# Kernel optimization log

Hardware: AMD Instinct MI355X
Metric: run time of the kernel (lower is better)

Reference implementation:

```python
import jax, jax.numpy as jnp
import numpy as np

N = 100000      # nodes
E = 800000      # edges (avg degree 8)
D_IN = 64
H1 = H2 = H3 = 64
HEADS = 2
D_EDGE = 5
NEG_SLOPE = 0.2  # GATConv leaky_relu slope


def _lin(key, fi, fo):
    kw, kb = jax.random.split(key)
    w = jax.random.normal(kw, (fi, fo), jnp.float32) / np.sqrt(fi)
    b = jax.random.normal(kb, (fo,), jnp.float32) * 0.01
    return w, b


def setup_inputs() -> dict:
    key = jax.random.key(0)
    ks = jax.random.split(key, 16)
    x = jax.random.normal(ks[0], (N, D_IN), jnp.float32)
    edge_index = jax.random.randint(ks[1], (2, E), 0, N, dtype=jnp.int32)
    edge_attr = jax.random.normal(ks[2], (E, D_EDGE), jnp.float32)

    inp = {"x": x, "edge_index": edge_index, "edge_attr": edge_attr}
    dims = [(D_IN, H1), (H1, H2), (H2, H3)]
    for i, (fi, fo) in enumerate(dims, start=1):
        k = jax.random.fold_in(ks[3], i)
        ka, kb, kc = jax.random.split(k, 3)
        inp[f"w_node{i}"], inp[f"b_node{i}"] = _lin(ka, fi, fo)
        inp[f"w_edge{i}"], inp[f"b_edge{i}"] = _lin(kb, D_EDGE, fo)
        inp[f"w_comb{i}"], inp[f"b_comb{i}"] = _lin(kc, 2 * fo, fo)
    # GATConv: shared lin for src/dst, att vectors, bias (concat=False -> size H3)
    kg, ks_, kd, kbias = jax.random.split(ks[4], 4)
    inp["w_gat"] = jax.random.normal(kg, (H3, HEADS * H3), jnp.float32) / np.sqrt(H3)
    inp["att_src"] = jax.random.normal(ks_, (HEADS, H3), jnp.float32) * 0.1
    inp["att_dst"] = jax.random.normal(kd, (HEADS, H3), jnp.float32) * 0.1
    inp["b_gat"] = jax.random.normal(kbias, (H3,), jnp.float32) * 0.01
    return inp


def _edge_conv(h, src, dst, ea, wn, bn, we, be, wc, bc, n):
    # lin_node / lin_edge applied densely, then gather -> concat -> lin -> scatter-add
    hn = h @ wn + bn                       # [N, C]
    ef = ea @ we + be                      # [E, C]
    msg = jnp.concatenate([hn[src], ef], axis=1) @ wc + bc  # [E, C]
    return jax.ops.segment_sum(msg, dst, num_segments=n)


def _gat(h, src, dst, w_gat, att_src, att_dst, b_gat, n):
    g = (h @ w_gat).reshape(n, HEADS, -1)          # [N, H, C]
    a_src = jnp.einsum("nhc,hc->nh", g, att_src)    # [N, H]
    a_dst = jnp.einsum("nhc,hc->nh", g, att_dst)
    alpha = jax.nn.leaky_relu(a_src[src] + a_dst[dst], NEG_SLOPE)  # [E, H]
    # segment softmax over incoming edges of each dst node
    m = jax.ops.segment_max(alpha, dst, num_segments=n)
    alpha = jnp.exp(alpha - m[dst])
    denom = jax.ops.segment_sum(alpha, dst, num_segments=n)
    alpha = alpha / (denom[dst] + 1e-16)
    out = jax.ops.segment_sum(g[src] * alpha[:, :, None], dst, num_segments=n)  # [N,H,C]
    return out.mean(axis=1) + b_gat  # concat=False -> mean over heads, plus bias


def reference(x, edge_index, edge_attr,
              w_node1, b_node1, w_edge1, b_edge1, w_comb1, b_comb1,
              w_node2, b_node2, w_edge2, b_edge2, w_comb2, b_comb2,
              w_node3, b_node3, w_edge3, b_edge3, w_comb3, b_comb3,
              w_gat, att_src, att_dst, b_gat):
    n = x.shape[0]
    src, dst = edge_index[0], edge_index[1]
    h = x
    h = jax.nn.relu(_edge_conv(h, src, dst, edge_attr, w_node1, b_node1, w_edge1, b_edge1, w_comb1, b_comb1, n))
    h = jax.nn.relu(_edge_conv(h, src, dst, edge_attr, w_node2, b_node2, w_edge2, b_edge2, w_comb2, b_comb2, n))
    h = jax.nn.relu(_edge_conv(h, src, dst, edge_attr, w_node3, b_node3, w_edge3, b_edge3, w_comb3, b_comb3, n))
    h = _gat(h, src, dst, w_gat, att_src, att_dst, b_gat, n)
    return h.reshape(-1)  # torch.flatten
```

## Files before the change

### kernel.cpp

```cpp
#include <hip/hip_runtime.h>
#include <hip/hip_fp16.h>
#include <math.h>


#define TPB 256

typedef unsigned int u32;

__device__ inline float2 f16unpack2(u32 u) {
    __half2 h = *reinterpret_cast<__half2*>(&u);
    return __half22float2(h);
}
__device__ inline float4 f16unpack4(uint2 q) {
    float2 a = f16unpack2(q.x), b = f16unpack2(q.y);
    return make_float4(a.x, a.y, b.x, b.y);
}
__device__ inline u32 f16pack2(float lo, float hi) {
    __half2 h = __floats2half2_rn(lo, hi);
    return *reinterpret_cast<u32*>(&h);
}
__device__ inline void acc_h16(float4& acc, uint2 v) {
    float2 a = f16unpack2(v.x);
    float2 b = f16unpack2(v.y);
    acc.x += a.x; acc.y += a.y; acc.z += b.x; acc.w += b.y;
}

#define MAC4(acc, a, w0, w1, w2, w3)                                           \
    acc.x = fmaf(a.x, w0.x, acc.x); acc.y = fmaf(a.x, w0.y, acc.y);            \
    acc.z = fmaf(a.x, w0.z, acc.z); acc.w = fmaf(a.x, w0.w, acc.w);            \
    acc.x = fmaf(a.y, w1.x, acc.x); acc.y = fmaf(a.y, w1.y, acc.y);            \
    acc.z = fmaf(a.y, w1.z, acc.z); acc.w = fmaf(a.y, w1.w, acc.w);            \
    acc.x = fmaf(a.z, w2.x, acc.x); acc.y = fmaf(a.z, w2.y, acc.y);            \
    acc.z = fmaf(a.z, w2.z, acc.z); acc.w = fmaf(a.z, w2.w, acc.w);            \
    acc.x = fmaf(a.w, w3.x, acc.x); acc.y = fmaf(a.w, w3.y, acc.y);            \
    acc.z = fmaf(a.w, w3.z, acc.z); acc.w = fmaf(a.w, w3.w, acc.w);

struct CombPtrs {
    const float* wn; const float* bn;
    const float* we; const float* be;
    const float* wc; const float* bc;
    float* W1;
};

__global__ __launch_bounds__(TPB) void k_prep(CombPtrs p0, CombPtrs p1, CombPtrs p2,
                                              const float* __restrict__ wg, u32* __restrict__ wgh,
                                              const float* __restrict__ att_src,
                                              const float* __restrict__ att_dst,
                                              float* __restrict__ vsd,
                                              const float4* __restrict__ X, uint4* __restrict__ XH,
                                              int n8, int nbC,
                                              int* __restrict__ rs, int nz) {
    const int b = blockIdx.x;
    if (b >= 4 + nbC) {
        int i = (b - 4 - nbC) * TPB + threadIdx.x;
        if (i < nz) rs[i] = 0;
        return;
    }
    if (b >= 4) {
        int i = (b - 4) * TPB + threadIdx.x;
        if (i < n8) {
            float4 a = X[i * 2], c = X[i * 2 + 1];
            uint4 o;
            o.x = f16pack2(a.x, a.y); o.y = f16pack2(a.z, a.w);
            o.z = f16pack2(c.x, c.y); o.w = f16pack2(c.z, c.w);
            XH[i] = o;
        }
        return;
    }
    if (b == 3) {
        for (int i = threadIdx.x; i < 4096; i += TPB) {
            float2 v = *(const float2*)&wg[i * 2];
            wgh[i] = f16pack2(v.x, v.y);
        }
        {
            int i = threadIdx.x;
            int type = i >> 6, k = i & 63;
            int h = type & 1, sd = type >> 1;
            const float* att = (sd ? att_dst : att_src) + h * 64;
            const float* wrow = wg + k * 128 + h * 64;
            float acc = 0.f;
            #pragma unroll 8
            for (int c = 0; c < 64; c++) acc = fmaf(wrow[c], att[c], acc);
            vsd[type * 64 + k] = acc;
        }
        return;
    }
    CombPtrs P = (b == 0) ? p0 : ((b == 1) ? p1 : p2);
    const float* wn = P.wn; const float* bn = P.bn;
    const float* we = P.we; const float* be = P.be;
    const float* wc = P.wc; const float* bc = P.bc;
    float* W1 = P.W1;
    float* W2 = P.W1 + 4096;
    float* cv = P.W1 + 4416;
    int tid = threadIdx.x;
    for (int idx = tid; idx < 64 * 64; idx += TPB) {
        int i = idx >> 6, j = idx & 63;
        float acc = 0.f;
        #pragma unroll 8
        for (int k = 0; k < 64; k++) acc = fmaf(wn[i * 64 + k], wc[k * 64 + j], acc);
        W1[idx] = acc;
    }
    for (int idx = tid; idx < 5 * 64; idx += TPB) {
        int i = idx >> 6, j = idx & 63;
        float acc = 0.f;
        #pragma unroll 8
        for (int k = 0; k < 64; k++) acc = fmaf(we[i * 64 + k], wc[(64 + k) * 64 + j], acc);
        W2[idx] = acc;
    }
    for (int j = tid; j < 64; j += TPB) {
        float acc = bc[j];
        for (int k = 0; k < 64; k++) {
            acc = fmaf(bn[k], wc[k * 64 + j], acc);
            acc = fmaf(be[k], wc[(64 + k) * 64 + j], acc);
        }
        cv[j] = acc;
    }
}

__global__ __launch_bounds__(TPB) void k_hist(const int* __restrict__ dst, int* __restrict__ cnt,
                                              int* __restrict__ rank, int E) {
    int e = blockIdx.x * TPB + threadIdx.x;
    if (e < E) rank[e] = atomicAdd(&cnt[dst[e]], 1);
}

__global__ __launch_bounds__(TPB) void k_scan1(int* __restrict__ data, int* __restrict__ partials, int n) {
    __shared__ int s[TPB];
    int i = blockIdx.x * TPB + threadIdx.x;
    int v = (i < n) ? data[i] : 0;
    s[threadIdx.x] = v;
    __syncthreads();
    for (int off = 1; off < TPB; off <<= 1) {
        int t = (threadIdx.x >= off) ? s[threadIdx.x - off] : 0;
        __syncthreads();
        s[threadIdx.x] += t;
        __syncthreads();
    }
    if (i < n) data[i] = s[threadIdx.x] - v;
    if (threadIdx.x == TPB - 1) partials[blockIdx.x] = s[TPB - 1];
}

__global__ __launch_bounds__(TPB) void k_scan3(int* __restrict__ data, const int* __restrict__ partials,
                                               int n, int total) {
    const int bid = blockIdx.x;
    int s = 0;
    for (int j = threadIdx.x; j < bid; j += TPB) s += partials[j];
    #pragma unroll
    for (int off = 32; off > 0; off >>= 1) s += __shfl_down(s, off);
    __shared__ int ws[4];
    if ((threadIdx.x & 63) == 0) ws[threadIdx.x >> 6] = s;
    __syncthreads();
    int pre = ws[0] + ws[1] + ws[2] + ws[3];
    int i = bid * TPB + threadIdx.x;
    if (i < n) data[i] += pre;
    if (i == 0) data[n] = total;
}

__global__ __launch_bounds__(TPB) void k_scatter(const int* __restrict__ src, const int* __restrict__ dst,
                                                 const int* __restrict__ rank, const int* __restrict__ row_start,
                                                 int2* __restrict__ csr_se, int E) {
    int e = blockIdx.x * TPB + threadIdx.x;
    if (e < E) {
        int idx = row_start[dst[e]] + rank[e];
        csr_se[idx] = make_int2(src[e], e);
    }
}

template <bool IN16, bool OUT16, bool SCORES, bool B5C>
__global__ __launch_bounds__(TPB, 6) void k_ec_fused(const void* __restrict__ Hv,
                                                     const int* __restrict__ row_start,
                                                     const int2* __restrict__ csr_se,
                                                     const float* __restrict__ Wfold,
                                                     float* __restrict__ B5,
                                                     const float* __restrict__ EA,
                                                     void* __restrict__ OUTv, int n,
                                                     const float* __restrict__ vsd,
                                                     float* __restrict__ asrc,
                                                     float* __restrict__ adst) {
    __shared__ float Alds[64 * 68];
    __shared__ float Blds[B5C ? 320 : 4];
    const float* Hf = (const float*)Hv;
    const u32*   Hh = (const u32*)Hv;
    const int t = threadIdx.x;
    const int base = blockIdx.x * 64;

    const int lane = t & 63;
    const int lid = lane & 15;
    const int gbase = lane & 48;
    const int gid = t >> 4;
    const int c4 = lid * 4;
    const int h2i = lid * 2;
    for (int i = 0; i < 4; i++) {
        int r = gid * 4 + i;
        int node = base + r;
        float4 acc = make_float4(0.f, 0.f, 0.f, 0.f);
        float b0 = 0.f, b1 = 0.f, b2 = 0.f, b3 = 0.f, b4 = 0.f;
        if (node < n) {
            int beg = row_start[node], end = row_start[node + 1];
            for (int chunk = beg; chunk < end; chunk += 16) {
                int cdeg = min(end - chunk, 16);
                bool ev = (chunk + lid < end);
                int2 se = ev ? csr_se[chunk + lid] : make_int2(0, 0);
                int s_l = se.x;
                if (B5C && ev) {
                    const float* p = EA + (size_t)se.y * 5;
                    b0 += p[0]; b1 += p[1]; b2 += p[2]; b3 += p[3]; b4 += p[4];
                }
                int it = 0;
                for (; it + 7 < cdeg; it += 8) {
                    int se0 = __shfl(s_l, gbase + it);
                    int se1 = __shfl(s_l, gbase + it + 1);
                    int se2 = __shfl(s_l, gbase + it + 2);
                    int se3 = __shfl(s_l, gbase + it + 3);
                    int se4 = __shfl(s_l, gbase + it + 4);
                    int se5 = __shfl(s_l, gbase + it + 5);
                    int se6 = __shfl(s_l, gbase + it + 6);
                    int se7 = __shfl(s_l, gbase + it + 7);
                    if (IN16) {
                        uint2 v0 = *(const uint2*)&Hh[(size_t)se0 * 32 + h2i];
                        uint2 v1 = *(const uint2*)&Hh[(size_t)se1 * 32 + h2i];
                        uint2 v2 = *(const uint2*)&Hh[(size_t)se2 * 32 + h2i];
                        uint2 v3 = *(const uint2*)&Hh[(size_t)se3 * 32 + h2i];
                        uint2 v4 = *(const uint2*)&Hh[(size_t)se4 * 32 + h2i];
                        uint2 v5 = *(const uint2*)&Hh[(size_t)se5 * 32 + h2i];
                        uint2 v6 = *(const uint2*)&Hh[(size_t)se6 * 32 + h2i];
                        uint2 v7 = *(const uint2*)&Hh[(size_t)se7 * 32 + h2i];
                        acc_h16(acc, v0); acc_h16(acc, v1); acc_h16(acc, v2); acc_h16(acc, v3);
                        acc_h16(acc, v4); acc_h16(acc, v5); acc_h16(acc, v6); acc_h16(acc, v7);
                    } else {
                        float4 v0 = *(const float4*)&Hf[(size_t)se0 * 64 + c4];
                        float4 v1 = *(const float4*)&Hf[(size_t)se1 * 64 + c4];
                        float4 v2 = *(const float4*)&Hf[(size_t)se2 * 64 + c4];
                        float4 v3 = *(const float4*)&Hf[(size_t)se3 * 64 + c4];
                        float4 v4 = *(const float4*)&Hf[(size_t)se4 * 64 + c4];
                        float4 v5 = *(const float4*)&Hf[(size_t)se5 * 64 + c4];
                        float4 v6 = *(const float4*)&Hf[(size_t)se6 * 64 + c4];
                        float4 v7 = *(const float4*)&Hf[(size_t)se7 * 64 + c4];
                        acc.x += ((v0.x + v1.x) + (v2.x + v3.x)) + ((v4.x + v5.x) + (v6.x + v7.x));
                        acc.y += ((v0.y + v1.y) + (v2.y + v3.y)) + ((v4.y + v5.y) + (v6.y + v7.y));
                        acc.z += ((v0.z + v1.z) + (v2.z + v3.z)) + ((v4.z + v5.z) + (v6.z + v7.z));
                        acc.w += ((v0.w + v1.w) + (v2.w + v3.w)) + ((v4.w + v5.w) + (v6.w + v7.w));
                    }
                }
                for (; it + 3 < cdeg; it += 4) {
                    int se0 = __shfl(s_l, gbase + it);
                    int se1 = __shfl(s_l, gbase + it + 1);
                    int se2 = __shfl(s_l, gbase + it + 2);
                    int se3 = __shfl(s_l, gbase + it + 3);
                    if (IN16) {
                        uint2 v0 = *(const uint2*)&Hh[(size_t)se0 * 32 + h2i];
                        uint2 v1 = *(const uint2*)&Hh[(size_t)se1 * 32 + h2i];
                        uint2 v2 = *(const uint2*)&Hh[(size_t)se2 * 32 + h2i];
                        uint2 v3 = *(const uint2*)&Hh[(size_t)se3 * 32 + h2i];
                        acc_h16(acc, v0); acc_h16(acc, v1); acc_h16(acc, v2); acc_h16(acc, v3);
                    } else {
                        float4 v0 = *(const float4*)&Hf[(size_t)se0 * 64 + c4];
                        float4 v1 = *(const float4*)&Hf[(size_t)se1 * 64 + c4];
                        float4 v2 = *(const float4*)&Hf[(size_t)se2 * 64 + c4];
                        float4 v3 = *(const float4*)&Hf[(size_t)se3 * 64 + c4];
                        acc.x += (v0.x + v1.x) + (v2.x + v3.x);
                        acc.y += (v0.y + v1.y) + (v2.y + v3.y);
                        acc.z += (v0.z + v1.z) + (v2.z + v3.z);
                        acc.w += (v0.w + v1.w) + (v2.w + v3.w);
                    }
                }
                for (; it < cdeg; it++) {
                    int se_ = __shfl(s_l, gbase + it);
                    if (IN16) {
                        uint2 v = *(const uint2*)&Hh[(size_t)se_ * 32 + h2i];
                        acc_h16(acc, v);
                    } else {
                        float4 v = *(const float4*)&Hf[(size_t)se_ * 64 + c4];
                        acc.x += v.x; acc.y += v.y; acc.z += v.z; acc.w += v.w;
                    }
                }
            }
        }
        *(float4*)&Alds[r * 68 + c4] = acc;
        if (B5C) {
            #pragma unroll
            for (int off = 1; off < 16; off <<= 1) {
                b0 += __shfl_xor(b0, off); b1 += __shfl_xor(b1, off);
                b2 += __shfl_xor(b2, off); b3 += __shfl_xor(b3, off);
                b4 += __shfl_xor(b4, off);
            }
            if (lid == 0 && node < n) {
                Blds[r * 5 + 0] = b0; Blds[r * 5 + 1] = b1; Blds[r * 5 + 2] = b2;
                Blds[r * 5 + 3] = b3; Blds[r * 5 + 4] = b4;
                float* bp = B5 + (size_t)node * 5;
                bp[0] = b0; bp[1] = b1; bp[2] = b2; bp[3] = b3; bp[4] = b4;
            }
        }
    }
    __syncthreads();

    const int r0 = (t >> 4) * 4, c0 = (t & 15) * 4;
    float4 acc0 = make_float4(0.f, 0.f, 0.f, 0.f), acc1 = acc0, acc2 = acc0, acc3 = acc0;
    #pragma unroll 2
    for (int k = 0; k < 64; k += 4) {
        float4 a0 = *(float4*)&Alds[(r0 + 0) * 68 + k];
        float4 a1 = *(float4*)&Alds[(r0 + 1) * 68 + k];
        float4 a2 = *(float4*)&Alds[(r0 + 2) * 68 + k];
        float4 a3 = *(float4*)&Alds[(r0 + 3) * 68 + k];
        float4 w0 = *(const float4*)&Wfold[(k + 0) * 64 + c0];
        float4 w1 = *(const float4*)&Wfold[(k + 1) * 64 + c0];
        float4 w2 = *(const float4*)&Wfold[(k + 2) * 64 + c0];
        float4 w3 = *(const float4*)&Wfold[(k + 3) * 64 + c0];
        MAC4(acc0, a0, w0, w1, w2, w3);
        MAC4(acc1, a1, w0, w1, w2, w3);
        MAC4(acc2, a2, w0, w1, w2, w3);
        MAC4(acc3, a3, w0, w1, w2, w3);
    }
    float4 w2c[5];
    #pragma unroll
    for (int j = 0; j < 5; j++) w2c[j] = *(const float4*)&Wfold[4096 + j * 64 + c0];
    const float4 cv4 = *(const float4*)&Wfold[4416 + c0];
    float4 vs0, vs1, vd0, vd1;
    if (SCORES) {
        vs0 = *(const float4*)&vsd[0 * 64 + c0];
        vs1 = *(const float4*)&vsd[1 * 64 + c0];
        vd0 = *(const float4*)&vsd[2 * 64 + c0];
        vd1 = *(const float4*)&vsd[3 * 64 + c0];
    }

    #define DOT4(a, b) (a.x * b.x + a.y * b.y + a.z * b.z + a.w * b.w)
    #define EC_STORE(i, acc)                                                        \
        { int row = base + r0 + i;                                                  \
          if (row < n) {                                                            \
              float deg = (float)(row_start[row + 1] - row_start[row]);             \
              float4 q;                                                             \
              q.x = deg * cv4.x; q.y = deg * cv4.y;                                 \
              q.z = deg * cv4.z; q.w = deg * cv4.w;                                 \
              for (int j = 0; j < 5; j++) {                                         \
                  float b = B5C ? Blds[(r0 + i) * 5 + j] : B5[(size_t)row * 5 + j]; \
                  q.x = fmaf(b, w2c[j].x, q.x); q.y = fmaf(b, w2c[j].y, q.y);       \
                  q.z = fmaf(b, w2c[j].z, q.z); q.w = fmaf(b, w2c[j].w, q.w);       \
              }                                                                     \
              float4 r4;                                                            \
              r4.x = fmaxf(acc.x + q.x, 0.f); r4.y = fmaxf(acc.y + q.y, 0.f);       \
              r4.z = fmaxf(acc.z + q.z, 0.f); r4.w = fmaxf(acc.w + q.w, 0.f);       \
              if (SCORES) {                                                         \
                  float s0 = DOT4(r4, vs0), s1 = DOT4(r4, vs1);                     \
                  float d0 = DOT4(r4, vd0), d1 = DOT4(r4, vd1);                     \
                  s0 += __shfl_xor(s0, 1); s1 += __shfl_xor(s1, 1);                 \
                  d0 += __shfl_xor(d0, 1); d1 += __shfl_xor(d1, 1);                 \
                  s0 += __shfl_xor(s0, 2); s1 += __shfl_xor(s1, 2);                 \
                  d0 += __shfl_xor(d0, 2); d1 += __shfl_xor(d1, 2);                 \
                  s0 += __shfl_xor(s0, 4); s1 += __shfl_xor(s1, 4);                 \
                  d0 += __shfl_xor(d0, 4); d1 += __shfl_xor(d1, 4);                 \
                  s0 += __shfl_xor(s0, 8); s1 += __shfl_xor(s1, 8);                 \
                  d0 += __shfl_xor(d0, 8); d1 += __shfl_xor(d1, 8);                 \
                  if ((t & 15) == 0) {                                              \
                      float2 sv; sv.x = s0; sv.y = s1;                              \
                      float2 dv; dv.x = d0; dv.y = d1;                              \
                      *(float2*)&asrc[(size_t)row * 2] = sv;                        \
                      *(float2*)&adst[(size_t)row * 2] = dv;                        \
                  }                                                                 \
              }                                                                     \
              if (OUT16) {                                                          \
                  u32* O = (u32*)OUTv;                                              \
                  uint2 gg;                                                         \
                  gg.x = f16pack2(r4.x, r4.y); gg.y = f16pack2(r4.z, r4.w);         \
                  *(uint2*)&O[(size_t)row * 32 + (c0 >> 1)] = gg;                   \
              } else {                                                              \
                  float* O = (float*)OUTv;                                          \
                  *(float4*)&O[(size_t)row * 64 + c0] = r4;                         \
              } } }
    EC_STORE(0, acc0) EC_STORE(1, acc1) EC_STORE(2, acc2) EC_STORE(3, acc3)
    #undef EC_STORE
    #undef DOT4
}

__global__ __launch_bounds__(TPB) void k_gat_agg(const u32* __restrict__ Hh,
                                                 const int* __restrict__ row_start,
                                                 const int2* __restrict__ csr_se,
                                                 const float* __restrict__ asrc,
                                                 const float* __restrict__ adst,
                                                 const u32* __restrict__ Wgh,
                                                 const float* __restrict__ bgat,
                                                 float* __restrict__ OUT, int n) {
    __shared__ float Ash[16][2][68];
    const int t = threadIdx.x;
    const int g = t >> 4;
    const int node = blockIdx.x * 16 + g;
    const int lane = t & 63;
    const int lid = lane & 15;
    const int gbase = lane & 48;
    const int h2i = lid * 2;
    const bool active = (node < n);

    float m0 = -INFINITY, m1 = -INFINITY, d0 = 0.f, d1 = 0.f;
    float A0[4] = {0.f, 0.f, 0.f, 0.f};
    float A1[4] = {0.f, 0.f, 0.f, 0.f};
    int beg = 0, end = 0;
    float2 adv = make_float2(0.f, 0.f);
    if (active) {
        beg = row_start[node]; end = row_start[node + 1];
        adv = *(const float2*)&adst[(size_t)node * 2];
    }
    for (int chunk = beg; chunk < end; chunk += 16) {
        int cdeg = min(end - chunk, 16);
        bool valid = (lid < cdeg);
        int s_l = valid ? csr_se[chunk + lid].x : 0;
        float al0 = -INFINITY, al1 = -INFINITY;
        if (valid) {
            float2 av = *(const float2*)&asrc[(size_t)s_l * 2];
            float t0 = av.x + adv.x, t1 = av.y + adv.y;
            al0 = (t0 > 0.f) ? t0 : 0.2f * t0;
            al1 = (t1 > 0.f) ? t1 : 0.2f * t1;
        }
        float cm0 = al0, cm1 = al1;
        #pragma unroll
        for (int off = 1; off < 16; off <<= 1) {
            cm0 = fmaxf(cm0, __shfl_xor(cm0, off));
            cm1 = fmaxf(cm1, __shfl_xor(cm1, off));
        }
        float nm0 = fmaxf(m0, cm0), nm1 = fmaxf(m1, cm1);
        float sc0 = __expf(m0 - nm0), sc1 = __expf(m1 - nm1);
        float w0 = valid ? __expf(al0 - nm0) : 0.f;
        float w1 = valid ? __expf(al1 - nm1) : 0.f;
        float cd0 = w0, cd1 = w1;
        #pragma unroll
        for (int off = 1; off < 16; off <<= 1) {
            cd0 += __shfl_xor(cd0, off);
            cd1 += __shfl_xor(cd1, off);
        }
        d0 = d0 * sc0 + cd0;
        d1 = d1 * sc1 + cd1;
        #pragma unroll
        for (int j = 0; j < 4; j++) { A0[j] *= sc0; A1[j] *= sc1; }
        m0 = nm0; m1 = nm1;
        int it = 0;
        for (; it + 3 < cdeg; it += 4) {
            int sa = __shfl(s_l, gbase + it);
            int sb = __shfl(s_l, gbase + it + 1);
            int sc = __shfl(s_l, gbase + it + 2);
            int sd = __shfl(s_l, gbase + it + 3);
            float w0a = __shfl(w0, gbase + it),     w1a = __shfl(w1, gbase + it);
            float w0b = __shfl(w0, gbase + it + 1), w1b = __shfl(w1, gbase + it + 1);
            float w0c = __shfl(w0, gbase + it + 2), w1c = __shfl(w1, gbase + it + 2);
            float w0d = __shfl(w0, gbase + it + 3), w1d = __shfl(w1, gbase + it + 3);
            float4 ha = f16unpack4(*(const uint2*)&Hh[(size_t)sa * 32 + h2i]);
            float4 hb = f16unpack4(*(const uint2*)&Hh[(size_t)sb * 32 + h2i]);
            float4 hc = f16unpack4(*(const uint2*)&Hh[(size_t)sc * 32 + h2i]);
            float4 hd = f16unpack4(*(const uint2*)&Hh[(size_t)sd * 32 + h2i]);
            A0[0] = fmaf(w0a, ha.x, A0[0]); A1[0] = fmaf(w1a, ha.x, A1[0]);
            A0[1] = fmaf(w0a, ha.y, A0[1]); A1[1] = fmaf(w1a, ha.y, A1[1]);
            A0[2] = fmaf(w0a, ha.z, A0[2]); A1[2] = fmaf(w1a, ha.z, A1[2]);
            A0[3] = fmaf(w0a, ha.w, A0[3]); A1[3] = fmaf(w1a, ha.w, A1[3]);
            A0[0] = fmaf(w0b, hb.x, A0[0]); A1[0] = fmaf(w1b, hb.x, A1[0]);
            A0[1] = fmaf(w0b, hb.y, A0[1]); A1[1] = fmaf(w1b, hb.y, A1[1]);
            A0[2] = fmaf(w0b, hb.z, A0[2]); A1[2] = fmaf(w1b, hb.z, A1[2]);
            A0[3] = fmaf(w0b, hb.w, A0[3]); A1[3] = fmaf(w1b, hb.w, A1[3]);
            A0[0] = fmaf(w0c, hc.x, A0[0]); A1[0] = fmaf(w1c, hc.x, A1[0]);
            A0[1] = fmaf(w0c, hc.y, A0[1]); A1[1] = fmaf(w1c, hc.y, A1[1]);
            A0[2] = fmaf(w0c, hc.z, A0[2]); A1[2] = fmaf(w1c, hc.z, A1[2]);
            A0[3] = fmaf(w0c, hc.w, A0[3]); A1[3] = fmaf(w1c, hc.w, A1[3]);
            A0[0] = fmaf(w0d, hd.x, A0[0]); A1[0] = fmaf(w1d, hd.x, A1[0]);
            A0[1] = fmaf(w0d, hd.y, A0[1]); A1[1] = fmaf(w1d, hd.y, A1[1]);
            A0[2] = fmaf(w0d, hd.z, A0[2]); A1[2] = fmaf(w1d, hd.z, A1[2]);
            A0[3] = fmaf(w0d, hd.w, A0[3]); A1[3] = fmaf(w1d, hd.w, A1[3]);
        }
        for (; it < cdeg; it++) {
            int sa = __shfl(s_l, gbase + it);
            float w0a = __shfl(w0, gbase + it), w1a = __shfl(w1, gbase + it);
            float4 ha = f16unpack4(*(const uint2*)&Hh[(size_t)sa * 32 + h2i]);
            A0[0] = fmaf(w0a, ha.x, A0[0]); A1[0] = fmaf(w1a, ha.x, A1[0]);
            A0[1] = fmaf(w0a, ha.y, A0[1]); A1[1] = fmaf(w1a, ha.y, A1[1]);
            A0[2] = fmaf(w0a, ha.z, A0[2]); A1[2] = fmaf(w1a, ha.z, A1[2]);
            A0[3] = fmaf(w0a, ha.w, A0[3]); A1[3] = fmaf(w1a, ha.w, A1[3]);
        }
    }
    float r0s = 0.5f / (d0 + 1e-16f);
    float r1s = 0.5f / (d1 + 1e-16f);
    #pragma unroll
    for (int j = 0; j < 4; j++) {
        Ash[g][0][lid * 4 + j] = A0[j] * r0s;
        Ash[g][1][lid * 4 + j] = A1[j] * r1s;
    }
    __syncthreads();

    if (active) {
        const int c0 = (t & 15) * 4;
        const float4 bg = *(const float4*)&bgat[c0];
        float4 acc = bg;
        #pragma unroll 4
        for (int k = 0; k < 64; k++) {
            float a0 = Ash[g][0][k];
            float a1 = Ash[g][1][k];
            float4 w0v = f16unpack4(*(const uint2*)&Wgh[k * 64 + (c0 >> 1)]);
            float4 w1v = f16unpack4(*(const uint2*)&Wgh[k * 64 + 32 + (c0 >> 1)]);
            acc.x = fmaf(a0, w0v.x, acc.x); acc.y = fmaf(a0, w0v.y, acc.y);
            acc.z = fmaf(a0, w0v.z, acc.z); acc.w = fmaf(a0, w0v.w, acc.w);
            acc.x = fmaf(a1, w1v.x, acc.x); acc.y = fmaf(a1, w1v.y, acc.y);
            acc.z = fmaf(a1, w1v.z, acc.z); acc.w = fmaf(a1, w1v.w, acc.w);
        }
        *(float4*)&OUT[(size_t)node * 64 + c0] = acc;
    }
}

extern "C" void kernel_launch(void* const* d_in, const int* in_sizes, int n_in,
                              void* d_out, int out_size, void* d_ws, size_t ws_size,
                              hipStream_t stream) {
    const float* x   = (const float*)d_in[0];
    const int*   ei  = (const int*)d_in[1];
    const float* ea  = (const float*)d_in[2];
    const int N = in_sizes[0] / 64;
    const int E = in_sizes[1] / 2;
    const int* src = ei;
    const int* dst = ei + E;

    const float* wn[3] = {(const float*)d_in[3],  (const float*)d_in[9],  (const float*)d_in[15]};
    const float* bn[3] = {(const float*)d_in[4],  (const float*)d_in[10], (const float*)d_in[16]};
    const float* we[3] = {(const float*)d_in[5],  (const float*)d_in[11], (const float*)d_in[17]};
    const float* be[3] = {(const float*)d_in[6],  (const float*)d_in[12], (const float*)d_in[18]};
    const float* wc[3] = {(const float*)d_in[7],  (const float*)d_in[13], (const float*)d_in[19]};
    const float* bc[3] = {(const float*)d_in[8],  (const float*)d_in[14], (const float*)d_in[20]};
    const float* wgat    = (const float*)d_in[21];
    const float* att_src = (const float*)d_in[22];
    const float* att_dst = (const float*)d_in[23];
    const float* bgat    = (const float*)d_in[24];

    char* ws = (char*)d_ws;
    size_t off = 0;
    auto alloc = [&](size_t bytes) -> void* {
        void* p = ws + off;
        off = (off + bytes + 255) & ~(size_t)255;
        return p;
    };
    int*   row_start = (int*)alloc((size_t)(N + 1) * 4);
    int*   partials  = (int*)alloc(1024 * 4);
    int*   rank      = (int*)alloc((size_t)E * 4);
    int2*  csr_se    = (int2*)alloc((size_t)E * 8);
    float* Wc        = (float*)alloc((size_t)3 * 4480 * 4);
    u32*   Wgh       = (u32*)alloc((size_t)4096 * 4);
    float* vsd       = (float*)alloc((size_t)256 * 4);
    float* B5        = (float*)alloc((size_t)N * 5 * 4);
    u32*   xh        = (u32*)alloc((size_t)N * 64 * 2);
    u32*   bufH0     = (u32*)alloc((size_t)N * 64 * 2);
    u32*   bufH1     = (u32*)alloc((size_t)N * 64 * 2);
    float* asrc      = (float*)alloc((size_t)N * 2 * 4);
    float* adst      = (float*)alloc((size_t)N * 2 * 4);
    float* out = (float*)d_out;

    const int nbN = (N + TPB - 1) / TPB;
    const int nbE = (E + TPB - 1) / TPB;
    const int grpBlocks = (N + 15) / 16;
    const int tiles = (N + 63) / 64;
    const int n8 = N * 8;
    const int nbC = (n8 + TPB - 1) / TPB;
    const int nbZ = (N + 1 + TPB - 1) / TPB;

    CombPtrs p0 = {wn[0], bn[0], we[0], be[0], wc[0], bc[0], Wc};
    CombPtrs p1 = {wn[1], bn[1], we[1], be[1], wc[1], bc[1], Wc + 4480};
    CombPtrs p2 = {wn[2], bn[2], we[2], be[2], wc[2], bc[2], Wc + 2 * 4480};
    k_prep<<<4 + nbC + nbZ, TPB, 0, stream>>>(p0, p1, p2, wgat, Wgh,
                                              att_src, att_dst, vsd,
                                              (const float4*)x, (uint4*)xh, n8, nbC,
                                              row_start, N + 1);

    k_hist<<<nbE, TPB, 0, stream>>>(dst, row_start, rank, E);
    k_scan1<<<nbN, TPB, 0, stream>>>(row_start, partials, N);
    k_scan3<<<nbN, TPB, 0, stream>>>(row_start, partials, N, E);
    k_scatter<<<nbE, TPB, 0, stream>>>(src, dst, rank, row_start, csr_se, E);

    k_ec_fused<true, true, false, true><<<tiles, TPB, 0, stream>>>(
        xh,    row_start, csr_se, Wc,            B5, ea, bufH0, N,
        nullptr, nullptr, nullptr);
    k_ec_fused<true, true, false, false><<<tiles, TPB, 0, stream>>>(
        bufH0, row_start, csr_se, Wc + 4480,     B5, nullptr, bufH1, N,
        nullptr, nullptr, nullptr);
    k_ec_fused<true, true, true, false><<<tiles, TPB, 0, stream>>>(
        bufH1, row_start, csr_se, Wc + 2 * 4480, B5, nullptr, bufH0, N,
        vsd, asrc, adst);

    k_gat_agg<<<grpBlocks, TPB, 0, stream>>>(bufH0, row_start, csr_se, asrc, adst,
                                             Wgh, bgat, out, N);
}
```

Before: 457.9 us.

## Tile GAT aggregation over 64 nodes per block with register-blocked output GEMM

The GAT aggregation kernel now handles 64 nodes per block, with each 16-lane group processing 4 nodes in sequence instead of one. Aggregated features are staged in shared memory as packed fp16, and the final per-head projection is register-blocked: each thread computes 4 rows × 4 columns, so each weight load is reused across four nodes. The gather loop is unrolled to 8 edges with all loads issued before the shuffles, and launch bounds request 6 blocks. The aim is to reduce redundant weight loads and expose more memory-level parallelism, at the cost of serialising nodes within a group and extra fp16 rounding of the intermediate.

```diff
diff --git a/kernel.cpp b/kernel.cpp
--- a/kernel.cpp
+++ b/kernel.cpp
@@ -370,132 +370,164 @@
     #undef DOT4
 }
 
-__global__ __launch_bounds__(TPB) void k_gat_agg(const u32* __restrict__ Hh,
-                                                 const int* __restrict__ row_start,
-                                                 const int2* __restrict__ csr_se,
-                                                 const float* __restrict__ asrc,
-                                                 const float* __restrict__ adst,
-                                                 const u32* __restrict__ Wgh,
-                                                 const float* __restrict__ bgat,
-                                                 float* __restrict__ OUT, int n) {
-    __shared__ float Ash[16][2][68];
+__global__ __launch_bounds__(TPB, 6) void k_gat_agg(const u32* __restrict__ Hh,
+                                                    const int* __restrict__ row_start,
+                                                    const int2* __restrict__ csr_se,
+                                                    const float* __restrict__ asrc,
+                                                    const float* __restrict__ adst,
+                                                    const u32* __restrict__ Wgh,
+                                                    const float* __restrict__ bgat,
+                                                    float* __restrict__ OUT, int n) {
+    __shared__ u32 Ash[64 * 66];
     const int t = threadIdx.x;
-    const int g = t >> 4;
-    const int node = blockIdx.x * 16 + g;
+    const int base = blockIdx.x * 64;
     const int lane = t & 63;
     const int lid = lane & 15;
     const int gbase = lane & 48;
+    const int gid = t >> 4;
     const int h2i = lid * 2;
-    const bool active = (node < n);
-
-    float m0 = -INFINITY, m1 = -INFINITY, d0 = 0.f, d1 = 0.f;
-    float A0[4] = {0.f, 0.f, 0.f, 0.f};
-    float A1[4] = {0.f, 0.f, 0.f, 0.f};
-    int beg = 0, end = 0;
-    float2 adv = make_float2(0.f, 0.f);
-    if (active) {
-        beg = row_start[node]; end = row_start[node + 1];
-        adv = *(const float2*)&adst[(size_t)node * 2];
-    }
-    for (int chunk = beg; chunk < end; chunk += 16) {
-        int cdeg = min(end - chunk, 16);
-        bool valid = (lid < cdeg);
-        int s_l = valid ? csr_se[chunk + lid].x : 0;
-        float al0 = -INFINITY, al1 = -INFINITY;
-        if (valid) {
-            float2 av = *(const float2*)&asrc[(size_t)s_l * 2];
-            float t0 = av.x + adv.x, t1 = av.y + adv.y;
-            al0 = (t0 > 0.f) ? t0 : 0.2f * t0;
-            al1 = (t1 > 0.f) ? t1 : 0.2f * t1;
+
+    #define EDGE_FMA(hv, wa0, wa1)                                              \
+        { float4 hx = f16unpack4(hv);                                           \
+          A0[0] = fmaf(wa0, hx.x, A0[0]); A1[0] = fmaf(wa1, hx.x, A1[0]);       \
+          A0[1] = fmaf(wa0, hx.y, A0[1]); A1[1] = fmaf(wa1, hx.y, A1[1]);       \
+          A0[2] = fmaf(wa0, hx.z, A0[2]); A1[2] = fmaf(wa1, hx.z, A1[2]);       \
+          A0[3] = fmaf(wa0, hx.w, A0[3]); A1[3] = fmaf(wa1, hx.w, A1[3]); }
+
+    for (int i = 0; i < 4; i++) {
+        int r = gid * 4 + i;
+        int node = base + r;
+        float m0 = -INFINITY, m1 = -INFINITY, d0 = 0.f, d1 = 0.f;
+        float A0[4] = {0.f, 0.f, 0.f, 0.f};
+        float A1[4] = {0.f, 0.f, 0.f, 0.f};
+        if (node < n) {
+            int beg = row_start[node], end = row_start[node + 1];
+            float2 adv = *(const float2*)&adst[(size_t)node * 2];
+            for (int chunk = beg; chunk < end; chunk += 16) {
+                int cdeg = min(end - chunk, 16);
+                bool valid = (lid < cdeg);
+                int s_l = valid ? csr_se[chunk + lid].x : 0;
+                float al0 = -INFINITY, al1 = -INFINITY;
+                if (valid) {
+                    float2 av = *(const float2*)&asrc[(size_t)s_l * 2];
+                    float t0 = av.x + adv.x, t1 = av.y + adv.y;
+                    al0 = (t0 > 0.f) ? t0 : 0.2f * t0;
+                    al1 = (t1 > 0.f) ? t1 : 0.2f * t1;
+                }
+                float cm0 = al0, cm1 = al1;
+                #pragma unroll
+                for (int off = 1; off < 16; off <<= 1) {
+                    cm0 = fmaxf(cm0, __shfl_xor(cm0, off));
+                    cm1 = fmaxf(cm1, __shfl_xor(cm1, off));
+                }
+                float nm0 = fmaxf(m0, cm0), nm1 = fmaxf(m1, cm1);
+                float sc0 = __expf(m0 - nm0), sc1 = __expf(m1 - nm1);
+                float w0 = valid ? __expf(al0 - nm0) : 0.f;
+                float w1 = valid ? __expf(al1 - nm1) : 0.f;
+                float cd0 = w0, cd1 = w1;
+                #pragma unroll
+                for (int off = 1; off < 16; off <<= 1) {
+                    cd0 += __shfl_xor(cd0, off);
+                    cd1 += __shfl_xor(cd1, off);
+                }
+                d0 = d0 * sc0 + cd0;
+                d1 = d1 * sc1 + cd1;
+                #pragma unroll
+                for (int j = 0; j < 4; j++) { A0[j] *= sc0; A1[j] *= sc1; }
+                m0 = nm0; m1 = nm1;
+                int it = 0;
+                for (; it + 7 < cdeg; it += 8) {
+                    int s0 = __shfl(s_l, gbase + it);
+                    int s1 = __shfl(s_l, gbase + it + 1);
+                    int s2 = __shfl(s_l, gbase + it + 2);
+                    int s3 = __shfl(s_l, gbase + it + 3);
+                    int s4 = __shfl(s_l, gbase + it + 4);
+                    int s5 = __shfl(s_l, gbase + it + 5);
+                    int s6 = __shfl(s_l, gbase + it + 6);
+                    int s7 = __shfl(s_l, gbase + it + 7);
+                    uint2 v0 = *(const uint2*)&Hh[(size_t)s0 * 32 + h2i];
+                    uint2 v1 = *(const uint2*)&Hh[(size_t)s1 * 32 + h2i];
+                    uint2 v2 = *(const uint2*)&Hh[(size_t)s2 * 32 + h2i];
+                    uint2 v3 = *(const uint2*)&Hh[(size_t)s3 * 32 + h2i];
+                    uint2 v4 = *(const uint2*)&Hh[(size_t)s4 * 32 + h2i];
+                    uint2 v5 = *(const uint2*)&Hh[(size_t)s5 * 32 + h2i];
+                    uint2 v6 = *(const uint2*)&Hh[(size_t)s6 * 32 + h2i];
+                    uint2 v7 = *(const uint2*)&Hh[(size_t)s7 * 32 + h2i];
+                    float w00 = __shfl(w0, gbase + it),     w10 = __shfl(w1, gbase + it);
+                    float w01 = __shfl(w0, gbase + it + 1), w11 = __shfl(w1, gbase + it + 1);
+                    float w02 = __shfl(w0, gbase + it + 2), w12 = __shfl(w1, gbase + it + 2);
+                    float w03 = __shfl(w0, gbase + it + 3), w13 = __shfl(w1, gbase + it + 3);
+                    float w04 = __shfl(w0, gbase + it + 4), w14 = __shfl(w1, gbase + it + 4);
+                    float w05 = __shfl(w0, gbase + it + 5), w15 = __shfl(w1, gbase + it + 5);
+                    float w06 = __shfl(w0, gbase + it + 6), w16 = __shfl(w1, gbase + it + 6);
+                    float w07 = __shfl(w0, gbase + it + 7), w17 = __shfl(w1, gbase + it + 7);
+                    EDGE_FMA(v0, w00, w10) EDGE_FMA(v1, w01, w11)
+                    EDGE_FMA(v2, w02, w12) EDGE_FMA(v3, w03, w13)
+                    EDGE_FMA(v4, w04, w14) EDGE_FMA(v5, w05, w15)
+                    EDGE_FMA(v6, w06, w16) EDGE_FMA(v7, w07, w17)
+                }
+                for (; it + 3 < cdeg; it += 4) {
+                    int s0 = __shfl(s_l, gbase + it);
+                    int s1 = __shfl(s_l, gbase + it + 1);
+                    int s2 = __shfl(s_l, gbase + it + 2);
+                    int s3 = __shfl(s_l, gbase + it + 3);
+                    uint2 v0 = *(const uint2*)&Hh[(size_t)s0 * 32 + h2i];
+                    uint2 v1 = *(const uint2*)&Hh[(size_t)s1 * 32 + h2i];
+                    uint2 v2 = *(const uint2*)&Hh[(size_t)s2 * 32 + h2i];
+                    uint2 v3 = *(const uint2*)&Hh[(size_t)s3 * 32 + h2i];
+                    float w00 = __shfl(w0, gbase + it),     w10 = __shfl(w1, gbase + it);
+                    float w01 = __shfl(w0, gbase + it + 1), w11 = __shfl(w1, gbase + it + 1);
+                    float w02 = __shfl(w0, gbase + it + 2), w12 = __shfl(w1, gbase + it + 2);
+                    float w03 = __shfl(w0, gbase + it + 3), w13 = __shfl(w1, gbase + it + 3);
+                    EDGE_FMA(v0, w00, w10) EDGE_FMA(v1, w01, w11)
+                    EDGE_FMA(v2, w02, w12) EDGE_FMA(v3, w03, w13)
+                }
+                for (; it < cdeg; it++) {
+                    int s0 = __shfl(s_l, gbase + it);
+                    uint2 v0 = *(const uint2*)&Hh[(size_t)s0 * 32 + h2i];
+                    float w00 = __shfl(w0, gbase + it), w10 = __shfl(w1, gbase + it);
+                    EDGE_FMA(v0, w00, w10)
+                }
+            }
         }
-        float cm0 = al0, cm1 = al1;
-        #pragma unroll
-        for (int off = 1; off < 16; off <<= 1) {
-            cm0 = fmaxf(cm0, __shfl_xor(cm0, off));
-            cm1 = fmaxf(cm1, __shfl_xor(cm1, off));
-        }
-        float nm0 = fmaxf(m0, cm0), nm1 = fmaxf(m1, cm1);
-        float sc0 = __expf(m0 - nm0), sc1 = __expf(m1 - nm1);
-        float w0 = valid ? __expf(al0 - nm0) : 0.f;
-        float w1 = valid ? __expf(al1 - nm1) : 0.f;
-        float cd0 = w0, cd1 = w1;
-        #pragma unroll
-        for (int off = 1; off < 16; off <<= 1) {
-            cd0 += __shfl_xor(cd0, off);
-            cd1 += __shfl_xor(cd1, off);
-        }
-        d0 = d0 * sc0 + cd0;
-        d1 = d1 * sc1 + cd1;
-        #pragma unroll
-        for (int j = 0; j < 4; j++) { A0[j] *= sc0; A1[j] *= sc1; }
-        m0 = nm0; m1 = nm1;
-        int it = 0;
-        for (; it + 3 < cdeg; it += 4) {
-            int sa = __shfl(s_l, gbase + it);
-            int sb = __shfl(s_l, gbase + it + 1);
-            int sc = __shfl(s_l, gbase + it + 2);
-            int sd = __shfl(s_l, gbase + it + 3);
-            float w0a = __shfl(w0, gbase + it),     w1a = __shfl(w1, gbase + it);
-            float w0b = __shfl(w0, gbase + it + 1), w1b = __shfl(w1, gbase + it + 1);
-            float w0c = __shfl(w0, gbase + it + 2), w1c = __shfl(w1, gbase + it + 2);
-            float w0d = __shfl(w0, gbase + it + 3), w1d = __shfl(w1, gbase + it + 3);
-            float4 ha = f16unpack4(*(const uint2*)&Hh[(size_t)sa * 32 + h2i]);
-            float4 hb = f16unpack4(*(const uint2*)&Hh[(size_t)sb * 32 + h2i]);
-            float4 hc = f16unpack4(*(const uint2*)&Hh[(size_t)sc * 32 + h2i]);
-            float4 hd = f16unpack4(*(const uint2*)&Hh[(size_t)sd * 32 + h2i]);
-            A0[0] = fmaf(w0a, ha.x, A0[0]); A1[0] = fmaf(w1a, ha.x, A1[0]);
-            A0[1] = fmaf(w0a, ha.y, A0[1]); A1[1] = fmaf(w1a, ha.y, A1[1]);
-            A0[2] = fmaf(w0a, ha.z, A0[2]); A1[2] = fmaf(w1a, ha.z, A1[2]);
-            A0[3] = fmaf(w0a, ha.w, A0[3]); A1[3] = fmaf(w1a, ha.w, A1[3]);
-            A0[0] = fmaf(w0b, hb.x, A0[0]); A1[0] = fmaf(w1b, hb.x, A1[0]);
-            A0[1] = fmaf(w0b, hb.y, A0[1]); A1[1] = fmaf(w1b, hb.y, A1[1]);
-            A0[2] = fmaf(w0b, hb.z, A0[2]); A1[2] = fmaf(w1b, hb.z, A1[2]);
-            A0[3] = fmaf(w0b, hb.w, A0[3]); A1[3] = fmaf(w1b, hb.w, A1[3]);
-            A0[0] = fmaf(w0c, hc.x, A0[0]); A1[0] = fmaf(w1c, hc.x, A1[0]);
-            A0[1] = fmaf(w0c, hc.y, A0[1]); A1[1] = fmaf(w1c, hc.y, A1[1]);
-            A0[2] = fmaf(w0c, hc.z, A0[2]); A1[2] = fmaf(w1c, hc.z, A1[2]);
-            A0[3] = fmaf(w0c, hc.w, A0[3]); A1[3] = fmaf(w1c, hc.w, A1[3]);
-            A0[0] = fmaf(w0d, hd.x, A0[0]); A1[0] = fmaf(w1d, hd.x, A1[0]);
-            A0[1] = fmaf(w0d, hd.y, A0[1]); A1[1] = fmaf(w1d, hd.y, A1[1]);
-            A0[2] = fmaf(w0d, hd.z, A0[2]); A1[2] = fmaf(w1d, hd.z, A1[2]);
-            A0[3] = fmaf(w0d, hd.w, A0[3]); A1[3] = fmaf(w1d, hd.w, A1[3]);
-        }
-        for (; it < cdeg; it++) {
-            int sa = __shfl(s_l, gbase + it);
-            float w0a = __shfl(w0, gbase + it), w1a = __shfl(w1, gbase + it);
-            float4 ha = f16unpack4(*(const uint2*)&Hh[(size_t)sa * 32 + h2i]);
-            A0[0] = fmaf(w0a, ha.x, A0[0]); A1[0] = fmaf(w1a, ha.x, A1[0]);
-            A0[1] = fmaf(w0a, ha.y, A0[1]); A1[1] = fmaf(w1a, ha.y, A1[1]);
-            A0[2] = fmaf(w0a, ha.z, A0[2]); A1[2] = fmaf(w1a, ha.z, A1[2]);
-            A0[3] = fmaf(w0a, ha.w, A0[3]); A1[3] = fmaf(w1a, ha.w, A1[3]);
-        }
-    }
-    float r0s = 0.5f / (d0 + 1e-16f);
-    float r1s = 0.5f / (d1 + 1e-16f);
-    #pragma unroll
-    for (int j = 0; j < 4; j++) {
-        Ash[g][0][lid * 4 + j] = A0[j] * r0s;
-        Ash[g][1][lid * 4 + j] = A1[j] * r1s;
-    }
+        float r0s = 0.5f / (d0 + 1e-16f);
+        float r1s = 0.5f / (d1 + 1e-16f);
+        Ash[r * 66 + h2i]          = f16pack2(A0[0] * r0s, A0[1] * r0s);
+        Ash[r * 66 + h2i + 1]      = f16pack2(A0[2] * r0s, A0[3] * r0s);
+        Ash[r * 66 + 32 + h2i]     = f16pack2(A1[0] * r1s, A1[1] * r1s);
+        Ash[r * 66 + 32 + h2i + 1] = f16pack2(A1[2] * r1s, A1[3] * r1s);
+    }
+    #undef EDGE_FMA
     __syncthreads();
 
-    if (active) {
-        const int c0 = (t & 15) * 4;
-        const float4 bg = *(const float4*)&bgat[c0];
-        float4 acc = bg;
-        #pragma unroll 4
-        for (int k = 0; k < 64; k++) {
-            float a0 = Ash[g][0][k];
-            float a1 = Ash[g][1][k];
-            float4 w0v = f16unpack4(*(const uint2*)&Wgh[k * 64 + (c0 >> 1)]);
-            float4 w1v = f16unpack4(*(const uint2*)&Wgh[k * 64 + 32 + (c0 >> 1)]);
-            acc.x = fmaf(a0, w0v.x, acc.x); acc.y = fmaf(a0, w0v.y, acc.y);
-            acc.z = fmaf(a0, w0v.z, acc.z); acc.w = fmaf(a0, w0v.w, acc.w);
-            acc.x = fmaf(a1, w1v.x, acc.x); acc.y = fmaf(a1, w1v.y, acc.y);
-            acc.z = fmaf(a1, w1v.z, acc.z); acc.w = fmaf(a1, w1v.w, acc.w);
-        }
-        *(float4*)&OUT[(size_t)node * 64 + c0] = acc;
-    }
+    const int r0 = (t >> 4) * 4, c0 = (t & 15) * 4;
+    const float4 bg = *(const float4*)&bgat[c0];
+    float4 acc0 = bg, acc1 = bg, acc2 = bg, acc3 = bg;
+    #pragma unroll 4
+    for (int kk = 0; kk < 32; kk++) {
+        float4 w0e = f16unpack4(*(const uint2*)&Wgh[(2 * kk)     * 64 + (c0 >> 1)]);
+        float4 w0o = f16unpack4(*(const uint2*)&Wgh[(2 * kk + 1) * 64 + (c0 >> 1)]);
+        float4 w1e = f16unpack4(*(const uint2*)&Wgh[(2 * kk)     * 64 + 32 + (c0 >> 1)]);
+        float4 w1o = f16unpack4(*(const uint2*)&Wgh[(2 * kk + 1) * 64 + 32 + (c0 >> 1)]);
+        #define GA_ROW(j, accj)                                                     \
+            { float2 a0 = f16unpack2(Ash[(r0 + j) * 66 + kk]);                      \
+              float2 a1 = f16unpack2(Ash[(r0 + j) * 66 + 32 + kk]);                 \
+              accj.x = fmaf(a0.x, w0e.x, accj.x); accj.y = fmaf(a0.x, w0e.y, accj.y); \
+              accj.z = fmaf(a0.x, w0e.z, accj.z); accj.w = fmaf(a0.x, w0e.w, accj.w); \
+              accj.x = fmaf(a0.y, w0o.x, accj.x); accj.y = fmaf(a0.y, w0o.y, accj.y); \
+              accj.z = fmaf(a0.y, w0o.z, accj.z); accj.w = fmaf(a0.y, w0o.w, accj.w); \
+              accj.x = fmaf(a1.x, w1e.x, accj.x); accj.y = fmaf(a1.x, w1e.y, accj.y); \
+              accj.z = fmaf(a1.x, w1e.z, accj.z); accj.w = fmaf(a1.x, w1e.w, accj.w); \
+              accj.x = fmaf(a1.y, w1o.x, accj.x); accj.y = fmaf(a1.y, w1o.y, accj.y); \
+              accj.z = fmaf(a1.y, w1o.z, accj.z); accj.w = fmaf(a1.y, w1o.w, accj.w); }
+        GA_ROW(0, acc0) GA_ROW(1, acc1) GA_ROW(2, acc2) GA_ROW(3, acc3)
+        #undef GA_ROW
+    }
+    #define GA_STORE(j, accj)                                                   \
+        { int row = base + r0 + j;                                              \
+          if (row < n) *(float4*)&OUT[(size_t)row * 64 + c0] = accj; }
+    GA_STORE(0, acc0) GA_STORE(1, acc1) GA_STORE(2, acc2) GA_STORE(3, acc3)
+    #undef GA_STORE
 }
 
 extern "C" void kernel_launch(void* const* d_in, const int* in_sizes, int n_in,
@@ -544,7 +576,6 @@
 
     const int nbN = (N + TPB - 1) / TPB;
     const int nbE = (E + TPB - 1) / TPB;
-    const int grpBlocks = (N + 15) / 16;
     const int tiles = (N + 63) / 64;
     const int n8 = N * 8;
     const int nbC = (n8 + TPB - 1) / TPB;
@@ -573,6 +604,6 @@
         bufH1, row_start, csr_se, Wc + 2 * 4480, B5, nullptr, bufH0, N,
         vsd, asrc, adst);
 
-    k_gat_agg<<<grpBlocks, TPB, 0, stream>>>(bufH0, row_start, csr_se, asrc, adst,
-                                             Wgh, bgat, out, N);
-}
+    k_gat_agg<<<tiles, TPB, 0, stream>>>(bufH0, row_start, csr_se, asrc, adst,
+                                         Wgh, bgat, out, N);
+}
```

New measurement: 421.3 us. 8.0% less time.
